# Kernel tuning notes

Measured on AMD Instinct MI355X. Metric: run time of the kernel, lower is better.

## Reference

```python
import jax, jax.numpy as jnp
import numpy as np

DIM = 512
HEADS = 8
HD = DIM // HEADS
HIDDEN = 4 * DIM
EPS = 1e-5


def layernorm(x, g, b):
    mu = jnp.mean(x, axis=-1, keepdims=True)
    var = jnp.mean(jnp.square(x - mu), axis=-1, keepdims=True)
    return (x - mu) * jax.lax.rsqrt(var + EPS) * g + b


def setup_inputs() -> dict:
    key = jax.random.key(0)
    ks = jax.random.split(key, 10)
    B, P, N, C = 16, 4, 256, DIM
    s = 1.0 / np.sqrt(C)
    sh = 1.0 / np.sqrt(HIDDEN)
    return {
        "x": jax.random.normal(ks[0], (B, P, N, C), jnp.float32),
        "ln1_g": jnp.ones((C,), jnp.float32),
        "ln1_b": jnp.zeros((C,), jnp.float32),
        "w_qkv": jax.random.uniform(ks[1], (3 * C, C), jnp.float32, -s, s),
        "w_proj": jax.random.uniform(ks[2], (C, C), jnp.float32, -s, s),
        "b_proj": jax.random.uniform(ks[3], (C,), jnp.float32, -s, s),
        "ln2_g": jnp.ones((C,), jnp.float32),
        "ln2_b": jnp.zeros((C,), jnp.float32),
        "w1": jax.random.uniform(ks[4], (HIDDEN, C), jnp.float32, -s, s),
        "b1": jax.random.uniform(ks[5], (HIDDEN,), jnp.float32, -s, s),
        "w2": jax.random.uniform(ks[6], (C, HIDDEN), jnp.float32, -sh, sh),
        "b2": jax.random.uniform(ks[7], (C,), jnp.float32, -sh, sh),
    }


def reference(x, ln1_g, ln1_b, w_qkv, w_proj, b_proj, ln2_g, ln2_b, w1, b1, w2, b2):
    B, P, N, C = x.shape
    # --- attention branch (batched over B, P, heads; same math as the unrolled loops) ---
    h = layernorm(x, ln1_g, ln1_b)
    qkv = jnp.einsum('bpnc,dc->bpnd', h, w_qkv)            # [B,P,N,3C]
    qkv = qkv.reshape(B, P, N, 3, HEADS, HD)
    q, k, v = qkv[..., 0, :, :], qkv[..., 1, :, :], qkv[..., 2, :, :]  # [B,P,N,H,hd]
    scale = HD ** -0.5
    attn = jnp.einsum('bpnhd,bpmhd->bphnm', q * scale, k)  # [B,P,H,N,N]
    attn = jax.nn.softmax(attn, axis=-1)
    o = jnp.einsum('bphnm,bpmhd->bpnhd', attn, v).reshape(B, P, N, C)
    o = jnp.einsum('bpnc,dc->bpnd', o, w_proj) + b_proj
    x = x + o
    # --- MLP branch ---
    h = layernorm(x, ln2_g, ln2_b)
    h = jax.nn.gelu(jnp.einsum('bpnc,hc->bpnh', h, w1) + b1, approximate=False)
    h = jnp.einsum('bpnh,ch->bpnc', h, w2) + b2
    return x + h
```

## Files before the change

kernel.cpp:

```cpp
#include <hip/hip_runtime.h>

typedef __attribute__((ext_vector_type(8))) short short8;
typedef __attribute__((ext_vector_type(4))) float f32x4;
typedef __attribute__((ext_vector_type(4))) unsigned short u16x4;
typedef __attribute__((ext_vector_type(2))) unsigned int u32x2;
typedef __attribute__((ext_vector_type(4))) unsigned int u32x4;

__device__ __forceinline__ float bf2f(unsigned short u) {
    return __uint_as_float(((unsigned)u) << 16);
}
__device__ __forceinline__ unsigned short f2bf(float f) {
    unsigned u = __float_as_uint(f);
    u += 0x7fffu + ((u >> 16) & 1u);
    return (unsigned short)(u >> 16);
}
__device__ __forceinline__ unsigned pack2(float a, float b) {
    unsigned r;
    asm("v_cvt_pk_bf16_f32 %0, %1, %2" : "=v"(r) : "v"(a), "v"(b));
    return r;
}
__device__ __forceinline__ void load_lds16(const void* g, void* l) {
    __builtin_amdgcn_global_load_lds(
        (const __attribute__((address_space(1))) void*)g,
        (__attribute__((address_space(3))) void*)l, 16, 0, 0);
}
__device__ __forceinline__ bool is_bf16(const unsigned* dt) {
    return *dt == 0x3F803F80u;
}
__device__ __forceinline__ float gelu_fast(float t) {
    float q = t * (1.5957691f + 0.07135482f * t * t);
    float e = __expf(-q);
    return __fdividef(t, 1.0f + e);
}

__global__ __launch_bounds__(512) void cast_all(
    const void* s_wqkv, const void* s_wproj, const void* s_w1, const void* s_w2,
    const void* v0, const void* v1, const void* v2, const void* v3,
    const void* v4, const void* v5, const void* v6,
    unsigned short* d_wqkv, unsigned short* d_wproj, unsigned short* d_w1,
    unsigned short* d_w2, unsigned short* par, const unsigned* dt)
{
    bool isbf = is_bf16(dt);
    int b = blockIdx.x, tid = threadIdx.x;
    if (b < 768) {
        const void* src; unsigned short* dst; int off;
        if (b < 192)      { src = s_wqkv;  dst = d_wqkv;  off = b * 4096; }
        else if (b < 256) { src = s_wproj; dst = d_wproj; off = (b - 192) * 4096; }
        else if (b < 512) { src = s_w1;    dst = d_w1;    off = (b - 256) * 4096; }
        else              { src = s_w2;    dst = d_w2;    off = (b - 512) * 4096; }
        int i = off + tid * 8;
        if (isbf) {
            *(short8*)(dst + i) = *(const short8*)((const unsigned short*)src + i);
        } else {
            const float* s = (const float*)src + i;
            short8 o;
            #pragma unroll
            for (int j = 0; j < 8; ++j) o[j] = (short)f2bf(s[j]);
            *(short8*)(dst + i) = o;
        }
    } else {
        const void* srcs[7]  = {v0, v1, v2, v3, v4, v5, v6};
        const int   sizes[7] = {512, 512, 512, 512, 512, 2048, 512};
        const int   offs[7]  = {0, 512, 1024, 1536, 2048, 2560, 4608};
        int j = b - 768;
        const void* s = srcs[j];
        unsigned short* d = par + offs[j];
        for (int i = tid; i < sizes[j]; i += 512)
            d[i] = isbf ? ((const unsigned short*)s)[i] : f2bf(((const float*)s)[i]);
    }
}

__global__ __launch_bounds__(256) void ln_kernel(
    const void* __restrict__ xin, size_t row0, int isf32,
    const unsigned short* __restrict__ g, const unsigned short* __restrict__ b,
    unsigned short* __restrict__ y)
{
    int w = threadIdx.x >> 6, lane = threadIdx.x & 63;
    size_t lr = (size_t)blockIdx.x * 4 + w;
    size_t gr = row0 + lr;
    float v[8];
    if (isf32) {
        const float* xr = (const float*)xin + (gr << 9) + (lane << 3);
        #pragma unroll
        for (int j = 0; j < 8; ++j) v[j] = xr[j];
    } else {
        short8 raw = *(const short8*)((const unsigned short*)xin + (gr << 9) + (lane << 3));
        #pragma unroll
        for (int j = 0; j < 8; ++j) v[j] = bf2f((unsigned short)raw[j]);
    }
    float sum = 0.f, sq = 0.f;
    #pragma unroll
    for (int j = 0; j < 8; ++j) { sum += v[j]; sq += v[j] * v[j]; }
    #pragma unroll
    for (int off = 32; off > 0; off >>= 1) {
        sum += __shfl_xor(sum, off);
        sq  += __shfl_xor(sq, off);
    }
    float mu  = sum * (1.0f / 512.0f);
    float var = sq * (1.0f / 512.0f) - mu * mu;
    float rs  = rsqrtf(var + 1e-5f);
    short8 gr8 = *(const short8*)(g + (lane << 3));
    short8 br8 = *(const short8*)(b + (lane << 3));
    float o[8];
    #pragma unroll
    for (int j = 0; j < 8; ++j)
        o[j] = (v[j] - mu) * rs * bf2f((unsigned short)gr8[j]) + bf2f((unsigned short)br8[j]);
    u32x4 ov = {pack2(o[0], o[1]), pack2(o[2], o[3]),
                pack2(o[4], o[5]), pack2(o[6], o[7])};
    *(u32x4*)(y + (lr << 9) + (lane << 3)) = ov;
}

__global__ __launch_bounds__(256, 2) void gemm_big(
    const unsigned short* __restrict__ A, const unsigned short* __restrict__ W,
    const unsigned short* __restrict__ bias,
    unsigned short* __restrict__ out,
    int NBY, int N, int K, int mode)
{
    __shared__ char lds[49152];

    int tid = threadIdx.x;
    int w = tid >> 6, lane = tid & 63;
    int l15 = lane & 15, g = lane >> 4;

    int L = blockIdx.x;
    int bx, by;
    if ((NBY & 7) == 0) {
        int nby8 = NBY >> 3;
        int xcd = L & 7, i = L >> 3;
        by = xcd * nby8 + (i % nby8);
        bx = i / nby8;
    } else {
        by = L % NBY;
        bx = L / NBY;
    }
    int m0 = by << 8, n0 = bx << 7;
    int wm = (w >> 1) << 7;
    int wn = (w & 1) << 6;

    int srow = tid >> 3;
    int u = (tid & 7) ^ (srow & 7);
    const unsigned short* gA[8];
    const unsigned short* gB[4];
    #pragma unroll
    for (int j = 0; j < 8; ++j)
        gA[j] = A + (size_t)(m0 + j * 32 + srow) * K + u * 8;
    #pragma unroll
    for (int j = 0; j < 4; ++j)
        gB[j] = W + (size_t)(n0 + j * 32 + srow) * K + u * 8;
    int lslot = tid * 16;
    int swz = l15 & 7;

    f32x4 acc[4][8];
    #pragma unroll
    for (int i = 0; i < 4; ++i)
        #pragma unroll
        for (int j = 0; j < 8; ++j) acc[i][j] = (f32x4){0.f, 0.f, 0.f, 0.f};

    for (int k = 0; k < K; k += 64) {
        if (k > 0) __syncthreads();
        #pragma unroll
        for (int j = 0; j < 8; ++j)
            load_lds16(gA[j] + k, &lds[j * 4096 + lslot]);
        #pragma unroll
        for (int j = 0; j < 4; ++j)
            load_lds16(gB[j] + k, &lds[32768 + j * 4096 + lslot]);
        __syncthreads();
        const char* bAct = lds;
        const char* bW = lds + 32768;
        #pragma unroll
        for (int s = 0; s < 2; ++s) {
            int cs = ((s * 4 + g) ^ swz) << 4;
            short8 wf[4];
            #pragma unroll
            for (int i = 0; i < 4; ++i)
                wf[i] = *(const short8*)(bW + (wn + i * 16 + l15) * 128 + cs);
            #pragma unroll
            for (int jg = 0; jg < 8; jg += 4) {
                short8 af[4];
                #pragma unroll
                for (int j = 0; j < 4; ++j)
                    af[j] = *(const short8*)(bAct + (wm + (jg + j) * 16 + l15) * 128 + cs);
                #pragma unroll
                for (int i = 0; i < 4; ++i)
                    #pragma unroll
                    for (int j = 0; j < 4; ++j)
                        acc[i][jg + j] = __builtin_amdgcn_mfma_f32_16x16x32_bf16(
                            wf[i], af[j], acc[i][jg + j], 0, 0, 0);
            }
        }
    }

    if (mode == 2) {
        #pragma unroll
        for (int i = 0; i < 4; ++i) {
            u16x4 bb = *(const u16x4*)(bias + n0 + wn + i * 16 + g * 4);
            #pragma unroll
            for (int j = 0; j < 8; ++j)
                #pragma unroll
                for (int r = 0; r < 4; ++r)
                    acc[i][j][r] = gelu_fast(acc[i][j][r] + bf2f(bb[r]));
        }
    }

    unsigned short* ob = out + (size_t)(m0 + wm + l15) * N + (n0 + wn + (g << 2));
    #pragma unroll
    for (int j = 0; j < 8; ++j) {
        unsigned short* orow = ob + (size_t)(j * 16) * N;
        #pragma unroll
        for (int i = 0; i < 4; ++i) {
            u32x2 pk = {pack2(acc[i][j][0], acc[i][j][1]),
                        pack2(acc[i][j][2], acc[i][j][3])};
            *(u32x2*)(orow + i * 16) = pk;
        }
    }
}

__global__ __launch_bounds__(256) void gemm8(
    const unsigned short* __restrict__ A, const unsigned short* __restrict__ W,
    const unsigned short* __restrict__ bias,
    const void* __restrict__ resid, size_t rrow0,
    void* __restrict__ out, size_t orow0,
    int NBY, int N, int K, int mode, int inbf)
{
    constexpr int BN = 128;
    __shared__ char lds[32768];

    int tid = threadIdx.x;
    int w = tid >> 6, lane = tid & 63;
    int l15 = lane & 15, g = lane >> 4;

    int L = blockIdx.x;
    int bx, by;
    if ((NBY & 7) == 0) {
        int nby8 = NBY >> 3;
        int xcd = L & 7, i = L >> 3;
        by = xcd * nby8 + (i % nby8);
        bx = i / nby8;
    } else {
        by = L % NBY;
        bx = L / NBY;
    }
    int m0 = by << 7, n0 = bx << 7;
    int wm = (w >> 1) << 6;
    int wn = (w & 1) << 6;

    int srow_t = tid >> 3;
    int u_t = (tid & 7) ^ (srow_t & 7);
    const unsigned short* gA[4];
    const unsigned short* gB[4];
    #pragma unroll
    for (int j = 0; j < 4; ++j) {
        gA[j] = A + (size_t)(m0 + j * 32 + srow_t) * K + u_t * 8;
        gB[j] = W + (size_t)(n0 + j * 32 + srow_t) * K + u_t * 8;
    }
    int lslot = tid * 16;
    int swz = l15 & 7;

    f32x4 acc[4][4];
    #pragma unroll
    for (int i = 0; i < 4; ++i)
        #pragma unroll
        for (int j = 0; j < 4; ++j) acc[i][j] = (f32x4){0.f, 0.f, 0.f, 0.f};

    for (int k = 0; k < K; k += 64) {
        if (k > 0) __syncthreads();
        #pragma unroll
        for (int j = 0; j < 4; ++j) {
            load_lds16(gA[j] + k, &lds[j * 4096 + lslot]);
            load_lds16(gB[j] + k, &lds[16384 + j * 4096 + lslot]);
        }
        __syncthreads();
        const char* bAct = lds;
        const char* bW = bAct + 16384;
        #pragma unroll
        for (int s = 0; s < 2; ++s) {
            int cs = ((s * 4 + g) ^ swz) << 4;
            short8 wf[4], af[4];
            #pragma unroll
            for (int i = 0; i < 4; ++i)
                wf[i] = *(const short8*)(bW + (wn + i * 16 + l15) * 128 + cs);
            #pragma unroll
            for (int j = 0; j < 4; ++j)
                af[j] = *(const short8*)(bAct + (wm + j * 16 + l15) * 128 + cs);
            #pragma unroll
            for (int i = 0; i < 4; ++i)
                #pragma unroll
                for (int j = 0; j < 4; ++j)
                    acc[i][j] = __builtin_amdgcn_mfma_f32_16x16x32_bf16(wf[i], af[j], acc[i][j], 0, 0, 0);
        }
    }
    __syncthreads();

    char* tb = (char*)lds;
    #pragma unroll
    for (int j = 0; j < 4; ++j) {
        int mloc = wm + j * 16 + l15;
        char* rowp = tb + mloc * (BN * 2);
        int sw = mloc & (BN / 4 - 2);
        #pragma unroll
        for (int i = 0; i < 4; ++i) {
            int cq = (wn + i * 16 + g * 4) >> 2;
            u32x2 pk = {pack2(acc[i][j][0], acc[i][j][1]),
                        pack2(acc[i][j][2], acc[i][j][3])};
            *(u32x2*)(rowp + ((cq ^ sw) << 3)) = pk;
        }
    }
    __syncthreads();

    int rL = tid >> 4;
    int lc = tid & 15;
    int colg = n0 + lc * 8;
    float bv[8];
    {
        short8 bb = *(const short8*)(bias + colg);
        #pragma unroll
        for (int t = 0; t < 8; ++t) bv[t] = bf2f((unsigned short)bb[t]);
    }

    #pragma unroll
    for (int ps = 0; ps < 8; ++ps) {
        int row = ps * 16 + rL;
        int rowL = m0 + row;
        int c16 = lc ^ ((row >> 1) & 15);
        short8 vv = *(const short8*)(tb + row * (BN * 2) + (c16 << 4));

        if (mode == 1) {
            size_t rbase = (rrow0 + rowL) * (size_t)N + colg;
            float o8[8];
            if (inbf) {
                short8 rr = *(const short8*)((const unsigned short*)resid + rbase);
                #pragma unroll
                for (int t = 0; t < 8; ++t)
                    o8[t] = bf2f((unsigned short)rr[t]) + bf2f((unsigned short)vv[t]) + bv[t];
            } else {
                f32x4 r0 = *(const f32x4*)((const float*)resid + rbase);
                f32x4 r1 = *(const f32x4*)((const float*)resid + rbase + 4);
                #pragma unroll
                for (int t = 0; t < 4; ++t) {
                    o8[t]     = r0[t] + bf2f((unsigned short)vv[t]) + bv[t];
                    o8[t + 4] = r1[t] + bf2f((unsigned short)vv[t + 4]) + bv[t + 4];
                }
            }
            u32x4 ov = {pack2(o8[0], o8[1]), pack2(o8[2], o8[3]),
                        pack2(o8[4], o8[5]), pack2(o8[6], o8[7])};
            *(u32x4*)((unsigned short*)out + (size_t)rowL * N + colg) = ov;
        } else {
            size_t rbase = (size_t)rowL * N + colg;
            short8 rr = *(const short8*)((const unsigned short*)resid + rbase);
            float o8[8];
            #pragma unroll
            for (int t = 0; t < 8; ++t)
                o8[t] = bf2f((unsigned short)rr[t]) + bf2f((unsigned short)vv[t]) + bv[t];
            size_t obase = (orow0 + rowL) * (size_t)N + colg;
            if (inbf) {
                u32x4 ov = {pack2(o8[0], o8[1]), pack2(o8[2], o8[3]),
                            pack2(o8[4], o8[5]), pack2(o8[6], o8[7])};
                *(u32x4*)((unsigned short*)out + obase) = ov;
            } else {
                float* ob = (float*)out + obase;
                *(f32x4*)ob       = (f32x4){o8[0], o8[1], o8[2], o8[3]};
                *(f32x4*)(ob + 4) = (f32x4){o8[4], o8[5], o8[6], o8[7]};
            }
        }
    }
}

__global__ __launch_bounds__(256) void attn_mfma(
    const unsigned short* __restrict__ qkv, unsigned short* __restrict__ o)
{
    __shared__ unsigned short Vt[64 * 256];
    __shared__ unsigned short Ps[4][16 * 256];
    int bp = blockIdx.x >> 3, h = blockIdx.x & 7;
    const unsigned short* base = qkv + (size_t)bp * 256 * 1536;
    int qo = h << 6, ko = 512 + (h << 6), vo = 1024 + (h << 6);
    int tid = threadIdx.x, w = tid >> 6, lane = tid & 63;
    int l15 = lane & 15, g = lane >> 4;

    {
        int d = tid & 63;
        for (int s = tid >> 6; s < 256; s += 4) {
            unsigned short v = base[(size_t)s * 1536 + vo + d];
            *(unsigned short*)((char*)Vt + d * 512 + (((s >> 3) ^ (d & 7)) << 4) + ((s & 7) << 1)) = v;
        }
    }
    __syncthreads();

    unsigned short* P = Ps[w];

    for (int pass = 0; pass < 4; ++pass) {
        int q0 = pass * 64 + w * 16;
        short8 qa[2];
        #pragma unroll
        for (int t = 0; t < 2; ++t)
            qa[t] = *(const short8*)(base + (size_t)(q0 + l15) * 1536 + qo + t * 32 + g * 8);
        f32x4 S[16];
        #pragma unroll
        for (int ns = 0; ns < 16; ++ns) {
            f32x4 a = {0.f, 0.f, 0.f, 0.f};
            #pragma unroll
            for (int t = 0; t < 2; ++t) {
                short8 kb = *(const short8*)(base + (size_t)(ns * 16 + l15) * 1536 + ko + t * 32 + g * 8);
                a = __builtin_amdgcn_mfma_f32_16x16x32_bf16(qa[t], kb, a, 0, 0, 0);
            }
            S[ns] = a;
        }
        float mx[4], sums[4], inv[4];
        #pragma unroll
        for (int r = 0; r < 4; ++r) {
            float m = -1e30f;
            #pragma unroll
            for (int ns = 0; ns < 16; ++ns) m = fmaxf(m, S[ns][r]);
            m *= 0.125f;
            #pragma unroll
            for (int off = 1; off < 16; off <<= 1) m = fmaxf(m, __shfl_xor(m, off));
            mx[r] = m;
            sums[r] = 0.f;
        }
        #pragma unroll
        for (int ns = 0; ns < 16; ++ns)
            #pragma unroll
            for (int r = 0; r < 4; ++r) {
                float p = __expf(S[ns][r] * 0.125f - mx[r]);
                sums[r] += p;
                S[ns][r] = p;
            }
        #pragma unroll
        for (int r = 0; r < 4; ++r) {
            float s2 = sums[r];
            #pragma unroll
            for (int off = 1; off < 16; off <<= 1) s2 += __shfl_xor(s2, off);
            inv[r] = 1.0f / s2;
        }
        #pragma unroll
        for (int ns = 0; ns < 16; ++ns)
            #pragma unroll
            for (int r = 0; r < 4; ++r) {
                int mq = g * 4 + r;
                int s = ns * 16 + l15;
                *(unsigned short*)((char*)P + mq * 512 + (((s >> 3) ^ (mq & 7)) << 4) + ((s & 7) << 1))
                    = f2bf(S[ns][r] * inv[r]);
            }
        f32x4 O[4];
        #pragma unroll
        for (int ds = 0; ds < 4; ++ds) O[ds] = (f32x4){0.f, 0.f, 0.f, 0.f};
        #pragma unroll
        for (int ks = 0; ks < 8; ++ks) {
            int c = (ks * 4 + g) ^ (l15 & 7);
            short8 pa = *(const short8*)((const char*)P + l15 * 512 + (c << 4));
            #pragma unroll
            for (int ds = 0; ds < 4; ++ds) {
                short8 vb = *(const short8*)((const char*)Vt + (ds * 16 + l15) * 512 + (c << 4));
                O[ds] = __builtin_amdgcn_mfma_f32_16x16x32_bf16(pa, vb, O[ds], 0, 0, 0);
            }
        }
        #pragma unroll
        for (int ds = 0; ds < 4; ++ds)
            #pragma unroll
            for (int r = 0; r < 4; ++r) {
                int mq = q0 + g * 4 + r;
                int d = ds * 16 + l15;
                o[((size_t)(bp * 256 + mq) << 9) + (h << 6) + d] = f2bf(O[ds][r]);
            }
    }
}

extern "C" void kernel_launch(void* const* d_in, const int* in_sizes, int n_in,
                              void* d_out, int out_size, void* d_ws, size_t ws_size,
                              hipStream_t stream)
{
    const void* x      = d_in[0];
    const void* ln1_g  = d_in[1];
    const void* ln1_b  = d_in[2];
    const void* w_qkv  = d_in[3];
    const void* w_proj = d_in[4];
    const void* b_proj = d_in[5];
    const void* ln2_g  = d_in[6];
    const void* ln2_b  = d_in[7];
    const void* w1     = d_in[8];
    const void* b1     = d_in[9];
    const void* w2     = d_in[10];
    const void* b2     = d_in[11];
    const unsigned* dt = (const unsigned*)ln1_g;

    const int isbf = (in_sizes[1] == 512 * 2);

    const int M = 16384;
    char* ws = (char*)d_ws;
    unsigned short* wqkv_b  = (unsigned short*)(ws);
    unsigned short* wproj_b = (unsigned short*)(ws + 1572864);
    unsigned short* w1_b    = (unsigned short*)(ws + 2097152);
    unsigned short* w2_b    = (unsigned short*)(ws + 4194304);
    unsigned short* par     = (unsigned short*)(ws + 6291456);
    const size_t CAST_END = 6308096;

    const unsigned short* p_wqkv  = isbf ? (const unsigned short*)w_qkv  : wqkv_b;
    const unsigned short* p_wproj = isbf ? (const unsigned short*)w_proj : wproj_b;
    const unsigned short* p_w1    = isbf ? (const unsigned short*)w1     : w1_b;
    const unsigned short* p_w2    = isbf ? (const unsigned short*)w2     : w2_b;
    const unsigned short* p_g1    = isbf ? (const unsigned short*)ln1_g  : par + 0;
    const unsigned short* p_b1ln  = isbf ? (const unsigned short*)ln1_b  : par + 512;
    const unsigned short* p_bproj = isbf ? (const unsigned short*)b_proj : par + 1024;
    const unsigned short* p_g2    = isbf ? (const unsigned short*)ln2_g  : par + 1536;
    const unsigned short* p_b2ln  = isbf ? (const unsigned short*)ln2_b  : par + 2048;
    const unsigned short* p_b1    = isbf ? (const unsigned short*)b1     : par + 2560;
    const unsigned short* p_b2    = isbf ? (const unsigned short*)b2     : par + 4608;

    int NC = 64;
    const int cand[7] = {1, 2, 4, 8, 16, 32, 64};
    for (int i = 0; i < 7; ++i) {
        size_t need = CAST_END + (size_t)(M / cand[i]) * 10240;
        if (need <= ws_size) { NC = cand[i]; break; }
    }
    const int R = M / NC;

    char* cb = ws + CAST_END;
    unsigned short* h   = (unsigned short*)(cb);
    unsigned short* qkv = (unsigned short*)(cb + (size_t)R * 1024);
    unsigned short* o   = (unsigned short*)(cb + (size_t)R * 4096);
    unsigned short* x2  = (unsigned short*)(cb + (size_t)R * 5120);
    unsigned short* hid = (unsigned short*)(cb + (size_t)R * 6144);
    unsigned short* h2  = h;

    if (!isbf) {
        cast_all<<<775, 512, 0, stream>>>(w_qkv, w_proj, w1, w2,
                                          ln1_g, ln1_b, b_proj, ln2_g, ln2_b, b1, b2,
                                          wqkv_b, wproj_b, w1_b, w2_b, par, dt);
    }

    for (int c = 0; c < NC; ++c) {
        const size_t r0 = (size_t)c * R;
        const int NBY  = R / 128;
        const int NBY2 = R / 256;

        ln_kernel<<<R / 4, 256, 0, stream>>>(x, r0, isbf ? 0 : 1, p_g1, p_b1ln, h);
        gemm_big<<<(1536 / 128) * NBY2, 256, 0, stream>>>(
            h, p_wqkv, nullptr, qkv, NBY2, 1536, 512, 0);
        attn_mfma<<<(R / 256) * 8, 256, 0, stream>>>(qkv, o);
        gemm8<<<(512 / 128) * NBY, 256, 0, stream>>>(
            o, p_wproj, p_bproj, x, r0, x2, 0, NBY, 512, 512, 1, isbf);
        ln_kernel<<<R / 4, 256, 0, stream>>>(x2, 0, 0, p_g2, p_b2ln, h2);
        gemm_big<<<(2048 / 128) * NBY2, 256, 0, stream>>>(
            h2, p_w1, p_b1, hid, NBY2, 2048, 512, 2);
        gemm8<<<(512 / 128) * NBY, 256, 0, stream>>>(
            hid, p_w2, p_b2, x2, 0, d_out, r0, NBY, 512, 2048, 3, isbf);
    }
}
```

Before: 321.8 us.

## Stage GEMM epilogue through swizzled LDS and hoist attention K fragments

Result: faster. 311.5 us (-3.2%).

```diff
diff --git a/kernel.cpp b/kernel.cpp
--- a/kernel.cpp
+++ b/kernel.cpp
@@ -189,6 +189,7 @@
             }
         }
     }
+    __syncthreads();
 
     if (mode == 2) {
         #pragma unroll
@@ -202,16 +203,35 @@
         }
     }
 
-    unsigned short* ob = out + (size_t)(m0 + wm + l15) * N + (n0 + wn + (g << 2));
-    #pragma unroll
-    for (int j = 0; j < 8; ++j) {
-        unsigned short* orow = ob + (size_t)(j * 16) * N;
-        #pragma unroll
-        for (int i = 0; i < 4; ++i) {
-            u32x2 pk = {pack2(acc[i][j][0], acc[i][j][1]),
-                        pack2(acc[i][j][2], acc[i][j][3])};
-            *(u32x2*)(orow + i * 16) = pk;
-        }
+    #pragma unroll
+    for (int hh = 0; hh < 2; ++hh) {
+        if ((w >> 1) == hh) {
+            #pragma unroll
+            for (int j = 0; j < 8; ++j) {
+                int mloc = j * 16 + l15;
+                char* rowp = lds + mloc * 256;
+                int sw = mloc & 30;
+                #pragma unroll
+                for (int i = 0; i < 4; ++i) {
+                    int cq = (wn + i * 16 + g * 4) >> 2;
+                    u32x2 pk = {pack2(acc[i][j][0], acc[i][j][1]),
+                                pack2(acc[i][j][2], acc[i][j][3])};
+                    *(u32x2*)(rowp + ((cq ^ sw) << 3)) = pk;
+                }
+            }
+        }
+        __syncthreads();
+        int rL = tid >> 4, lc = tid & 15;
+        int colg = n0 + lc * 8;
+        #pragma unroll
+        for (int ps = 0; ps < 8; ++ps) {
+            int row = ps * 16 + rL;
+            int rowL = m0 + hh * 128 + row;
+            int c16 = lc ^ ((row >> 1) & 15);
+            short8 vv = *(const short8*)(lds + row * 256 + (c16 << 4));
+            *(short8*)(out + (size_t)rowL * N + colg) = vv;
+        }
+        if (hh == 0) __syncthreads();
     }
 }
 
@@ -385,6 +405,13 @@
     }
     __syncthreads();
 
+    short8 kb[16][2];
+    #pragma unroll
+    for (int ns = 0; ns < 16; ++ns)
+        #pragma unroll
+        for (int t = 0; t < 2; ++t)
+            kb[ns][t] = *(const short8*)(base + (size_t)(ns * 16 + l15) * 1536 + ko + t * 32 + g * 8);
+
     unsigned short* P = Ps[w];
 
     for (int pass = 0; pass < 4; ++pass) {
@@ -398,10 +425,8 @@
         for (int ns = 0; ns < 16; ++ns) {
             f32x4 a = {0.f, 0.f, 0.f, 0.f};
             #pragma unroll
-            for (int t = 0; t < 2; ++t) {
-                short8 kb = *(const short8*)(base + (size_t)(ns * 16 + l15) * 1536 + ko + t * 32 + g * 8);
-                a = __builtin_amdgcn_mfma_f32_16x16x32_bf16(qa[t], kb, a, 0, 0, 0);
-            }
+            for (int t = 0; t < 2; ++t)
+                a = __builtin_amdgcn_mfma_f32_16x16x32_bf16(qa[t], kb[ns][t], a, 0, 0, 0);
             S[ns] = a;
         }
         float mx[4], sums[4], inv[4];
```
